# Optimization experiments

Measured on AMD Instinct MI355X. Metric: run time of the kernel, lower is better.

## Reference

```python
import jax, jax.numpy as jnp
import numpy as np

B, S, D = 2, 2048, 2048
H, KVH, HD = 16, 8, 128          # heads, kv heads, head_dim
KVR = 512                        # kv_lora_rank
THETA, ROPE_FACTOR = 10000.0, 40.0
EPS = 1e-5
NEG = -1e9


def _layernorm(x, scale):
    mean = jnp.mean(x, axis=-1, keepdims=True)
    var = jnp.mean(jnp.square(x - mean), axis=-1, keepdims=True)
    return (x - mean) * jax.lax.rsqrt(var + EPS) * scale


def _rope_cos_sin(position_ids):
    # freqs over half the head dim, scaled by rope_factor (as in source)
    freqs = (1.0 / THETA ** (jnp.arange(0, HD, 2, dtype=jnp.float32) / HD)) * ROPE_FACTOR
    ang = position_ids.astype(jnp.float32)[:, None] * freqs[None, :]  # [S, HD//2]
    return jnp.cos(ang)[None, :, None, :], jnp.sin(ang)[None, :, None, :]


def _apply_rope(x, cos, sin):
    # x: [B,S,h,HD] with interleaved (real, imag) pairs
    x_ = x.reshape(*x.shape[:-1], -1, 2)
    xr, xi = x_[..., 0], x_[..., 1]
    out = jnp.stack([xr * cos - xi * sin, xr * sin + xi * cos], axis=-1)
    return out.reshape(x.shape)


def setup_inputs() -> dict:
    key = jax.random.key(0)
    ks = jax.random.split(key, 6)
    std = 0.02
    x = jax.random.normal(ks[0], (B, S, D), jnp.float32)
    wq = jax.random.normal(ks[1], (D, H * 2 * HD), jnp.float32) * std
    wkv_a = jax.random.normal(ks[2], (D, KVR + HD), jnp.float32) * std
    kv_norm_scale = jnp.ones((KVR,), jnp.float32)
    wkv_b = jax.random.normal(ks[3], (KVR, KVH * 2 * HD), jnp.float32) * std
    wo = jax.random.normal(ks[4], (H * HD, D), jnp.float32) * std
    causal = jnp.tril(jnp.ones((S, S), bool))
    attention_mask = jnp.where(causal, 0.0, NEG)[None, None].astype(jnp.float32)
    position_ids = jnp.arange(S, dtype=jnp.int32)
    return {"x": x, "wq": wq, "wkv_a": wkv_a, "kv_norm_scale": kv_norm_scale,
            "wkv_b": wkv_b, "wo": wo, "attention_mask": attention_mask,
            "position_ids": position_ids}


def reference(x, wq, wkv_a, kv_norm_scale, wkv_b, wo, attention_mask, position_ids):
    cos, sin = _rope_cos_sin(position_ids)
    # Q path: low-rank disabled (q_lora_rank=0) -> single projection
    q = (x @ wq).reshape(B, S, H, 2 * HD)
    q_nope, q_pe = q[..., :HD], q[..., HD:]
    q = jnp.concatenate([q_nope, _apply_rope(q_pe, cos, sin)], axis=-1)  # [B,S,H,2HD]
    # KV path: low-rank compression + decoupled rope key
    kv = x @ wkv_a                               # [B,S,KVR+HD]
    kv_c = _layernorm(kv[..., :KVR], kv_norm_scale)
    k_pe = kv[..., KVR:]                         # [B,S,HD]
    kvb = (kv_c @ wkv_b).reshape(B, S, KVH, 2 * HD)
    k_nope, v = kvb[..., :HD], kvb[..., HD:]
    k_pe = _apply_rope(k_pe[:, :, None, :], cos, sin)  # [B,S,1,HD]
    k = jnp.concatenate([k_nope, jnp.broadcast_to(k_pe, (B, S, KVH, HD))], axis=-1)
    # GQA expansion
    rep = H // KVH
    k = jnp.repeat(k, rep, axis=2)
    v = jnp.repeat(v, rep, axis=2)
    scale = HD ** -0.5
    scores = jnp.einsum('bqhd,bkhd->bhqk', q, k) * scale + attention_mask
    probs = jax.nn.softmax(scores, axis=-1)
    attn = jnp.einsum('bhqk,bkhd->bqhd', probs, v).reshape(B, S, H * HD)
    return attn @ wo
```

## Files before the change

### kernel.cpp

```cpp
#include <hip/hip_runtime.h>


typedef __attribute__((ext_vector_type(8))) short short8;
typedef __attribute__((ext_vector_type(4))) float floatx4;
typedef unsigned short u16;
typedef unsigned int u32;

__device__ __forceinline__ float bf2f(u16 u){ u32 x=((u32)u)<<16; return __builtin_bit_cast(float,x); }
__device__ __forceinline__ u16 f2bf(float f){ u32 x=__builtin_bit_cast(u32,f); return (u16)((x + 0x7fffu + ((x>>16)&1u))>>16); }

__device__ __forceinline__ floatx4 mfma16(short8 a, short8 b, floatx4 c){
  return __builtin_amdgcn_mfma_f32_16x16x32_bf16(a,b,c,0,0,0);
}

__device__ __forceinline__ void gl_lds16(const u16* g, u16* l){
  __builtin_amdgcn_global_load_lds((const __attribute__((address_space(1))) void*)g,
                                   (__attribute__((address_space(3))) void*)l, 16, 0, 0);
}

__global__ __launch_bounds__(256)
void k_f2b(const float* __restrict__ in, u16* __restrict__ out, size_t n){
  size_t i = ((size_t)blockIdx.x*256 + threadIdx.x)*4;
  if(i >= n) return;
  float4 v = *(const float4*)(in + i);
  out[i+0] = f2bf(v.x); out[i+1] = f2bf(v.y); out[i+2] = f2bf(v.z); out[i+3] = f2bf(v.w);
}

__global__ void k_transpose(const float* __restrict__ in, u16* __restrict__ out, int K, int N){
  __shared__ u16 tile[32][33];
  const int kb = blockIdx.y*32, nb = blockIdx.x*32;
  const int tx = threadIdx.x, ty = threadIdx.y;
#pragma unroll
  for(int i=0;i<4;i++) tile[ty+i*8][tx] = f2bf(in[(size_t)(kb+ty+i*8)*N + nb + tx]);
  __syncthreads();
#pragma unroll
  for(int i=0;i<4;i++) out[(size_t)(nb+ty+i*8)*K + kb + tx] = tile[tx][ty+i*8];
}

__global__ void k_rope_table(float* __restrict__ cosT, float* __restrict__ sinT){
  int idx = blockIdx.x*256 + threadIdx.x;
  if(idx >= 2048*64) return;
  int p = idx>>6, i = idx&63;
  double freq = pow(10000.0, -(double)(2*i)/128.0) * 40.0;
  float ff = (float)freq;
  float ang = (float)((double)p * (double)ff);
  cosT[idx] = (float)cos((double)ang);
  sinT[idx] = (float)sin((double)ang);
}

template<int OUTF32>
__global__ __launch_bounds__(256)
void k_gemm_bt(const u16* __restrict__ A, const u16* __restrict__ Bt, void* __restrict__ Cout,
               int M, int N, int K){
  __shared__ __align__(16) u16 lsA[128*32];
  __shared__ __align__(16) u16 lsB[128*32];
  const int t = threadIdx.x;
  const int m0 = blockIdx.y*128, n0 = blockIdx.x*128;
  const int wv = t>>6, ln = t&63;
  const int wr = (wv>>1)*64, wc = (wv&1)*64;
  const int fr = ln&15, kh = (ln>>4)*8;
  const int srow = wv*16 + (ln>>2), sk = (ln&3)*8;
  const u16* Ag = A + (size_t)(m0 + srow)*K + sk;
  const u16* Bg = Bt + (size_t)(n0 + srow)*K + sk;
  u16* lA0 = &lsA[wv*512];
  u16* lB0 = &lsB[wv*512];
  floatx4 acc[4][4];
#pragma unroll
  for(int i=0;i<4;i++)
#pragma unroll
    for(int j=0;j<4;j++) acc[i][j] = (floatx4){0.f,0.f,0.f,0.f};
  for(int k0=0;k0<K;k0+=32){
    __syncthreads();
    gl_lds16(Ag + k0,              lA0);
    gl_lds16(Ag + (size_t)64*K + k0, lA0 + 2048);
    gl_lds16(Bg + k0,              lB0);
    gl_lds16(Bg + (size_t)64*K + k0, lB0 + 2048);
    __syncthreads();
    short8 af[4], bf[4];
#pragma unroll
    for(int i=0;i<4;i++) af[i] = *(const short8*)&lsA[(wr + i*16 + fr)*32 + kh];
#pragma unroll
    for(int i=0;i<4;i++) bf[i] = *(const short8*)&lsB[(wc + i*16 + fr)*32 + kh];
#pragma unroll
    for(int mi=0;mi<4;mi++)
#pragma unroll
      for(int ni=0;ni<4;ni++) acc[mi][ni] = mfma16(af[mi], bf[ni], acc[mi][ni]);
  }
  const int r0 = (ln>>4)*4, c0 = ln&15;
#pragma unroll
  for(int mi=0;mi<4;mi++)
#pragma unroll
    for(int ni=0;ni<4;ni++){
      const int row = m0 + wr + mi*16 + r0;
      const int col = n0 + wc + ni*16 + c0;
#pragma unroll
      for(int r=0;r<4;r++){
        float v = acc[mi][ni][r];
        if(OUTF32) ((float*)Cout)[(size_t)(row+r)*N + col] = v;
        else       ((u16*)Cout)[(size_t)(row+r)*N + col] = f2bf(v);
      }
    }
}

__global__ __launch_bounds__(256)
void k_ln_rope(const float* __restrict__ kv, const float* __restrict__ scale,
               const int* __restrict__ pid, const float* __restrict__ cosT,
               const float* __restrict__ sinT, u16* __restrict__ kv_cn, u16* __restrict__ k_pe){
  const int tok = blockIdx.x;
  const int t = threadIdx.x;
  const float* row = kv + (size_t)tok*640;
  float v0 = row[2*t], v1 = row[2*t+1];
  float s = v0+v1, ss = v0*v0+v1*v1;
#pragma unroll
  for(int off=32; off>=1; off>>=1){ s += __shfl_xor(s,off); ss += __shfl_xor(ss,off); }
  __shared__ float red[8];
  if((t&63)==0){ red[t>>6]=s; red[4+(t>>6)]=ss; }
  __syncthreads();
  float S4 = red[0]+red[1]+red[2]+red[3];
  float SS4 = red[4]+red[5]+red[6]+red[7];
  float mean = S4*(1.f/512.f);
  float var = SS4*(1.f/512.f) - mean*mean;
  float inv = rsqrtf(var + 1e-5f);
  kv_cn[(size_t)tok*512 + 2*t]   = f2bf((v0-mean)*inv*scale[2*t]);
  kv_cn[(size_t)tok*512 + 2*t+1] = f2bf((v1-mean)*inv*scale[2*t+1]);
  if(t < 128){
    const int sidx = tok & 2047;
    const int p = pid[sidx];
    const int i = t>>1;
    float c = cosT[p*64+i], sn = sinT[p*64+i];
    float xr = row[512+2*i], xi = row[512+2*i+1];
    float val = (t&1) ? (xr*sn + xi*c) : (xr*c - xi*sn);
    k_pe[(size_t)tok*128 + t] = f2bf(val);
  }
}

__global__ __launch_bounds__(256)
void k_q_rope(const u16* __restrict__ q_raw, const int* __restrict__ pid,
              const float* __restrict__ cosT, const float* __restrict__ sinT,
              u16* __restrict__ q_fin){
  const float QS = (float)(0.08838834764831845 * 1.4426950408889634);
  const int tok = blockIdx.x;
  const int b = tok>>11, sidx = tok&2047;
  const int t = threadIdx.x;
  const int p = pid[sidx];
  const int h = t>>4, seg = t&15;
  const u16* src = q_raw + (size_t)tok*4096 + h*256 + seg*16;
  u16* dst = q_fin + (((size_t)(b*16 + h))*2048 + sidx)*256 + seg*16;
  short8 a = *(const short8*)src;
  short8 bv = *(const short8*)(src+8);
  short8 oa, ob;
  if(seg < 8){
#pragma unroll
    for(int j=0;j<8;j++){
      oa[j] = (short)f2bf(bf2f((u16)a[j])*QS);
      ob[j] = (short)f2bf(bf2f((u16)bv[j])*QS);
    }
  } else {
    const int i0 = seg*8 - 64;
#pragma unroll
    for(int j=0;j<4;j++){
      float c = cosT[p*64 + i0 + j], sn = sinT[p*64 + i0 + j];
      float xr = bf2f((u16)a[2*j]), xi = bf2f((u16)a[2*j+1]);
      oa[2*j]   = (short)f2bf((xr*c - xi*sn)*QS);
      oa[2*j+1] = (short)f2bf((xr*sn + xi*c)*QS);
    }
#pragma unroll
    for(int j=0;j<4;j++){
      float c = cosT[p*64 + i0 + 4 + j], sn = sinT[p*64 + i0 + 4 + j];
      float xr = bf2f((u16)bv[2*j]), xi = bf2f((u16)bv[2*j+1]);
      ob[2*j]   = (short)f2bf((xr*c - xi*sn)*QS);
      ob[2*j+1] = (short)f2bf((xr*sn + xi*c)*QS);
    }
  }
  *(short8*)dst = oa;
  *(short8*)(dst+8) = ob;
}

__global__ __launch_bounds__(256)
void k_build_k(const u16* __restrict__ kvb, const u16* __restrict__ k_pe, u16* __restrict__ k_full){
  const int tok = blockIdx.x;
  const int b = tok>>11, sidx = tok&2047;
  const int t = threadIdx.x;
  const int kh = t>>5, seg = t&31;
  short8 v;
  if(seg < 16) v = *(const short8*)(kvb + (size_t)tok*2048 + kh*256 + seg*8);
  else         v = *(const short8*)(k_pe + (size_t)tok*128 + (seg-16)*8);
  *(short8*)(k_full + (((size_t)(b*8 + kh))*2048 + sidx)*256 + seg*8) = v;
}

__global__ void k_v_t(const u16* __restrict__ kvb, u16* __restrict__ v_t){
  __shared__ u16 tile[32][33];
  const int sb = blockIdx.x*32, hb = blockIdx.y*32;
  const int bk = blockIdx.z;
  const int b = bk>>3, kh = bk&7;
  const int tx = threadIdx.x, ty = threadIdx.y;
#pragma unroll
  for(int i=0;i<4;i++){
    int sidx = sb + ty + i*8;
    tile[ty+i*8][tx] = kvb[((size_t)(b*2048 + sidx))*2048 + kh*256 + 128 + hb + tx];
  }
  __syncthreads();
#pragma unroll
  for(int i=0;i<4;i++){
    int hd = hb + ty + i*8;
    v_t[(((size_t)bk*64 + blockIdx.x)*128 + hd)*32 + tx] = tile[tx][ty+i*8];
  }
}

__global__ __launch_bounds__(256, 3)
void k_attn(const u16* __restrict__ q_fin, const u16* __restrict__ k_full,
            const u16* __restrict__ v_t, u16* __restrict__ attn){
  __shared__ __align__(16) u16 lsK[2*8192];
  __shared__ __align__(16) u16 lsP[4*16*40];
  const int blk = blockIdx.x;
  const int kvh = blk&7;
  const int bb  = (blk>>3)&1;
  const int qr  = blk>>4;
  const int qt  = 31 - (qr>>1);
  const int h   = kvh*2 + (qr&1);
  const int t = threadIdx.x, wv = t>>6, ln = t&63;
  const int fq = ln&15, gq = ln>>4;
  const u16* kbase = k_full + ((size_t)(bb*8 + kvh))*2048*256;
  const u16* vbase = v_t + ((size_t)(bb*8 + kvh))*128*2048;
  u16* Pw = &lsP[wv*16*40];

  int soff[4];
#pragma unroll
  for(int s4=0;s4<4;s4++){
    int o = s4*4096 + wv*1024 + ln*16;
    int row = o>>9, colb = o&511;
    soff[s4] = row*512 + (colb ^ ((row&7)<<4));
  }
  const int swz = (fq&7)<<4;
  int cb[8];
#pragma unroll
  for(int c=0;c<8;c++) cb[c] = (gq*16 + c*64) ^ swz;
  const int rowb = fq*512;
  const u16* vfp = vbase + (size_t)fq*32 + gq*8;

  const int last = 2*qt + 1;
  short8 qf[8];
  const u16* qb = q_fin + (((size_t)(bb*16 + h))*2048 + qt*64 + wv*16 + fq)*256;
#pragma unroll
  for(int c=0;c<8;c++) qf[c] = *(const short8*)(qb + c*32 + gq*8);
  floatx4 oacc[8];
#pragma unroll
  for(int ii=0;ii<8;ii++) oacc[ii] = (floatx4){0.f,0.f,0.f,0.f};
  float mprev = -3e38f, lsum = 0.f;

#pragma unroll
  for(int s4=0;s4<4;s4++)
    gl_lds16((const u16*)((const char*)kbase + soff[s4]), &lsK[s4*2048 + wv*512]);
  __syncthreads();

  int cur = 0;
  for(int kt=0; kt<=last; kt++){
    if(kt < last){
      const char* ktile = (const char*)kbase + (size_t)(kt+1)*16384;
      u16* kdst = &lsK[(cur^1)*8192];
#pragma unroll
      for(int s4=0;s4<4;s4++)
        gl_lds16((const u16*)(ktile + soff[s4]), kdst + s4*2048 + wv*512);
    }
    short8 vf[8];
#pragma unroll
    for(int hs=0;hs<8;hs++)
      vf[hs] = *(const short8*)(vfp + (size_t)kt*4096 + hs*512);

    const char* Kc = (const char*)lsK + cur*16384;
    floatx4 sc[2];
#pragma unroll
    for(int ns=0;ns<2;ns++) sc[ns] = (floatx4){0.f,0.f,0.f,0.f};
#pragma unroll
    for(int ns=0;ns<2;ns++){
#pragma unroll
      for(int c=0;c<8;c++){
        short8 kf = *(const short8*)(Kc + ns*8192 + rowb + cb[c]);
        sc[ns] = mfma16(kf, qf[c], sc[ns]);
      }
    }
    if(kt >= 2*qt){
      const int off = (kt - 2*qt)*32;
      const int qloc = wv*16 + fq;
#pragma unroll
      for(int ns=0;ns<2;ns++)
#pragma unroll
        for(int r=0;r<4;r++)
          if(off + ns*16 + gq*4 + r > qloc) sc[ns][r] = -1e30f;
    }
    float mloc = -3e38f;
#pragma unroll
    for(int ns=0;ns<2;ns++)
#pragma unroll
      for(int r=0;r<4;r++) mloc = fmaxf(mloc, sc[ns][r]);
    mloc = fmaxf(mloc, __shfl_xor(mloc, 16));
    mloc = fmaxf(mloc, __shfl_xor(mloc, 32));
    if(__any(mloc > mprev + 8.f)){
      const float mn = fmaxf(mprev, mloc);
      const float alpha = exp2f(mprev - mn);
      lsum *= alpha;
      float alphaO[4];
#pragma unroll
      for(int r=0;r<4;r++) alphaO[r] = __shfl(alpha, gq*4 + r);
#pragma unroll
      for(int hs=0;hs<8;hs++)
#pragma unroll
        for(int r=0;r<4;r++) oacc[hs][r] *= alphaO[r];
      mprev = mn;
    }
    float ps = 0.f;
#pragma unroll
    for(int ns=0;ns<2;ns++)
#pragma unroll
      for(int r=0;r<4;r++){
        float p = exp2f(sc[ns][r] - mprev);
        sc[ns][r] = p;
        ps += p;
      }
    ps += __shfl_xor(ps, 16);
    ps += __shfl_xor(ps, 32);
    lsum += ps;

#pragma unroll
    for(int ns=0;ns<2;ns++){
      u32 p01, p23;
      asm("v_cvt_pk_bf16_f32 %0, %1, %2" : "=v"(p01) : "v"(sc[ns][0]), "v"(sc[ns][1]));
      asm("v_cvt_pk_bf16_f32 %0, %1, %2" : "=v"(p23) : "v"(sc[ns][2]), "v"(sc[ns][3]));
      uint2 pk; pk.x = p01; pk.y = p23;
      *(uint2*)&Pw[fq*40 + ns*16 + gq*4] = pk;
    }
    __builtin_amdgcn_s_waitcnt(0xC07F);

    short8 pa = *(const short8*)&Pw[fq*40 + gq*8];
#pragma unroll
    for(int hs=0;hs<8;hs++)
      oacc[hs] = mfma16(pa, vf[hs], oacc[hs]);

    __syncthreads();
    cur ^= 1;
  }
  const float inv = 1.f / lsum;
  float invO[4];
#pragma unroll
  for(int r=0;r<4;r++) invO[r] = __shfl(inv, gq*4 + r);
#pragma unroll
  for(int hs=0;hs<8;hs++)
#pragma unroll
    for(int r=0;r<4;r++){
      const int qi = qt*64 + wv*16 + gq*4 + r;
      attn[(((size_t)(bb*2048 + qi))*16 + h)*128 + hs*16 + fq] = f2bf(oacc[hs][r]*invO[r]);
    }
}

extern "C" void kernel_launch(void* const* d_in, const int* in_sizes, int n_in,
                              void* d_out, int out_size, void* d_ws, size_t ws_size,
                              hipStream_t stream){
  const float* x    = (const float*)d_in[0];
  const float* wq   = (const float*)d_in[1];
  const float* wkva = (const float*)d_in[2];
  const float* kvsc = (const float*)d_in[3];
  const float* wkvb = (const float*)d_in[4];
  const float* wo   = (const float*)d_in[5];
  const int* pid  = (const int*)d_in[7];
  float* out = (float*)d_out;

  char* w = (char*)d_ws;
  size_t off = 0;
  auto alloc = [&](size_t bytes)->void*{
    void* p = (void*)(w + off);
    off += (bytes + 255) & ~(size_t)255;
    return p;
  };
  u16*   x_bf   = (u16*)alloc((size_t)4096*2048*2);
  u16*   wq_t   = (u16*)alloc((size_t)4096*2048*2);
  u16*   wkva_t = (u16*)alloc((size_t)640*2048*2);
  u16*   wkvb_t = (u16*)alloc((size_t)2048*512*2);
  u16*   wo_t   = (u16*)alloc((size_t)2048*2048*2);
  float* cosT   = (float*)alloc((size_t)2048*64*4);
  float* sinT   = (float*)alloc((size_t)2048*64*4);
  u16*   q_raw  = (u16*)alloc((size_t)4096*4096*2);
  float* kvf    = (float*)alloc((size_t)4096*640*4);
  u16*   kv_cn  = (u16*)alloc((size_t)4096*512*2);
  u16*   k_pe   = (u16*)alloc((size_t)4096*128*2);
  u16*   kvb    = (u16*)alloc((size_t)4096*2048*2);
  u16*   q_fin  = (u16*)alloc((size_t)4096*4096*2);
  u16*   k_full = (u16*)alloc((size_t)2*8*2048*256*2);
  u16*   v_t    = (u16*)alloc((size_t)2*8*128*2048*2);
  u16*   attn   = (u16*)alloc((size_t)4096*2048*2);

  k_f2b<<<8192, 256, 0, stream>>>(x, x_bf, (size_t)4096*2048);
  k_transpose<<<dim3(128, 64), dim3(32,8), 0, stream>>>(wq,   wq_t,   2048, 4096);
  k_transpose<<<dim3(20,  64), dim3(32,8), 0, stream>>>(wkva, wkva_t, 2048, 640);
  k_transpose<<<dim3(64,  16), dim3(32,8), 0, stream>>>(wkvb, wkvb_t, 512,  2048);
  k_transpose<<<dim3(64,  64), dim3(32,8), 0, stream>>>(wo,   wo_t,   2048, 2048);
  k_rope_table<<<512, 256, 0, stream>>>(cosT, sinT);

  k_gemm_bt<0><<<dim3(32, 32), 256, 0, stream>>>(x_bf, wq_t, q_raw, 4096, 4096, 2048);
  k_gemm_bt<1><<<dim3(5,  32), 256, 0, stream>>>(x_bf, wkva_t, kvf, 4096, 640, 2048);
  k_ln_rope<<<4096, 256, 0, stream>>>(kvf, kvsc, pid, cosT, sinT, kv_cn, k_pe);
  k_gemm_bt<0><<<dim3(16, 32), 256, 0, stream>>>(kv_cn, wkvb_t, kvb, 4096, 2048, 512);
  k_q_rope<<<4096, 256, 0, stream>>>(q_raw, pid, cosT, sinT, q_fin);
  k_build_k<<<4096, 256, 0, stream>>>(kvb, k_pe, k_full);
  k_v_t<<<dim3(64, 4, 16), dim3(32,8), 0, stream>>>(kvb, v_t);
  k_attn<<<1024, 256, 0, stream>>>(q_fin, k_full, v_t, attn);
  k_gemm_bt<1><<<dim3(16, 32), 256, 0, stream>>>(attn, wo_t, out, 4096, 2048, 2048);
}
```

Measured before the change: 517.9 us.

## Use 2-wave attention blocks with two 16-row query tiles per wave

The attention kernel now runs 128 threads (2 waves) per block instead of 4. Each wave handles 32 query rows as two 16-row sub-tiles, so each K fragment read from LDS and each V fragment loaded from global memory feeds twice as many MFMAs. The block-to-tile mapping also changes to interleave short and long causal query tiles (0..7, 31..24, 8..15, 23..16), which should balance load across the grid. The cost is roughly double the accumulator and Q registers per wave and a lower occupancy bound, which may hurt latency hiding.

```diff
diff --git a/kernel.cpp b/kernel.cpp
--- a/kernel.cpp
+++ b/kernel.cpp
@@ -207,29 +207,37 @@
   }
 }
 
-__global__ __launch_bounds__(256, 3)
+__global__ __launch_bounds__(128, 2)
 void k_attn(const u16* __restrict__ q_fin, const u16* __restrict__ k_full,
             const u16* __restrict__ v_t, u16* __restrict__ attn){
   __shared__ __align__(16) u16 lsK[2*8192];
-  __shared__ __align__(16) u16 lsP[4*16*40];
+  __shared__ __align__(16) u16 lsP[2*32*40];
   const int blk = blockIdx.x;
   const int kvh = blk&7;
-  const int bb  = (blk>>3)&1;
-  const int qr  = blk>>4;
-  const int qt  = 31 - (qr>>1);
-  const int h   = kvh*2 + (qr&1);
+  const int i  = blk>>3;
+  const int j  = i>>5;
+  const int mm = i&31;
+  const int s  = mm>>2;
+  int qt;
+  if(j==0)      qt = s;
+  else if(j==1) qt = 31 - s;
+  else if(j==2) qt = 8 + s;
+  else          qt = 23 - s;
+  const int bb = (mm>>1)&1;
+  const int hp = mm&1;
+  const int h  = kvh*2 + hp;
   const int t = threadIdx.x, wv = t>>6, ln = t&63;
   const int fq = ln&15, gq = ln>>4;
   const u16* kbase = k_full + ((size_t)(bb*8 + kvh))*2048*256;
   const u16* vbase = v_t + ((size_t)(bb*8 + kvh))*128*2048;
-  u16* Pw = &lsP[wv*16*40];
-
-  int soff[4];
-#pragma unroll
-  for(int s4=0;s4<4;s4++){
-    int o = s4*4096 + wv*1024 + ln*16;
+  u16* Pw = &lsP[wv*32*40];
+
+  int soff[8];
+#pragma unroll
+  for(int s8=0;s8<8;s8++){
+    int o = s8*2048 + t*16;
     int row = o>>9, colb = o&511;
-    soff[s4] = row*512 + (colb ^ ((row&7)<<4));
+    soff[s8] = row*512 + (colb ^ ((row&7)<<4));
   }
   const int swz = (fq&7)<<4;
   int cb[8];
@@ -239,18 +247,23 @@
   const u16* vfp = vbase + (size_t)fq*32 + gq*8;
 
   const int last = 2*qt + 1;
-  short8 qf[8];
-  const u16* qb = q_fin + (((size_t)(bb*16 + h))*2048 + qt*64 + wv*16 + fq)*256;
-#pragma unroll
-  for(int c=0;c<8;c++) qf[c] = *(const short8*)(qb + c*32 + gq*8);
-  floatx4 oacc[8];
-#pragma unroll
-  for(int ii=0;ii<8;ii++) oacc[ii] = (floatx4){0.f,0.f,0.f,0.f};
-  float mprev = -3e38f, lsum = 0.f;
-
-#pragma unroll
-  for(int s4=0;s4<4;s4++)
-    gl_lds16((const u16*)((const char*)kbase + soff[s4]), &lsK[s4*2048 + wv*512]);
+  short8 qf[2][8];
+#pragma unroll
+  for(int m=0;m<2;m++){
+    const u16* qb = q_fin + (((size_t)(bb*16 + h))*2048 + qt*64 + wv*32 + m*16 + fq)*256;
+#pragma unroll
+    for(int c=0;c<8;c++) qf[m][c] = *(const short8*)(qb + c*32 + gq*8);
+  }
+  floatx4 oacc[2][8];
+#pragma unroll
+  for(int m=0;m<2;m++)
+#pragma unroll
+    for(int ii=0;ii<8;ii++) oacc[m][ii] = (floatx4){0.f,0.f,0.f,0.f};
+  float mprev0 = -3e38f, mprev1 = -3e38f, lsum0 = 0.f, lsum1 = 0.f;
+
+#pragma unroll
+  for(int s8=0;s8<8;s8++)
+    gl_lds16((const u16*)((const char*)kbase + soff[s8]), &lsK[s8*1024 + wv*512]);
   __syncthreads();
 
   int cur = 0;
@@ -259,8 +272,8 @@
       const char* ktile = (const char*)kbase + (size_t)(kt+1)*16384;
       u16* kdst = &lsK[(cur^1)*8192];
 #pragma unroll
-      for(int s4=0;s4<4;s4++)
-        gl_lds16((const u16*)(ktile + soff[s4]), kdst + s4*2048 + wv*512);
+      for(int s8=0;s8<8;s8++)
+        gl_lds16((const u16*)(ktile + soff[s8]), kdst + s8*1024 + wv*512);
     }
     short8 vf[8];
 #pragma unroll
@@ -268,88 +281,102 @@
       vf[hs] = *(const short8*)(vfp + (size_t)kt*4096 + hs*512);
 
     const char* Kc = (const char*)lsK + cur*16384;
-    floatx4 sc[2];
-#pragma unroll
-    for(int ns=0;ns<2;ns++) sc[ns] = (floatx4){0.f,0.f,0.f,0.f};
+    floatx4 sc[2][2];
+#pragma unroll
+    for(int m=0;m<2;m++)
+#pragma unroll
+      for(int ns=0;ns<2;ns++) sc[m][ns] = (floatx4){0.f,0.f,0.f,0.f};
 #pragma unroll
     for(int ns=0;ns<2;ns++){
 #pragma unroll
       for(int c=0;c<8;c++){
         short8 kf = *(const short8*)(Kc + ns*8192 + rowb + cb[c]);
-        sc[ns] = mfma16(kf, qf[c], sc[ns]);
+        sc[0][ns] = mfma16(kf, qf[0][c], sc[0][ns]);
+        sc[1][ns] = mfma16(kf, qf[1][c], sc[1][ns]);
       }
     }
     if(kt >= 2*qt){
       const int off = (kt - 2*qt)*32;
-      const int qloc = wv*16 + fq;
-#pragma unroll
-      for(int ns=0;ns<2;ns++)
-#pragma unroll
-        for(int r=0;r<4;r++)
-          if(off + ns*16 + gq*4 + r > qloc) sc[ns][r] = -1e30f;
-    }
-    float mloc = -3e38f;
+#pragma unroll
+      for(int m=0;m<2;m++){
+        const int qloc = wv*32 + m*16 + fq;
+#pragma unroll
+        for(int ns=0;ns<2;ns++)
+#pragma unroll
+          for(int r=0;r<4;r++)
+            if(off + ns*16 + gq*4 + r > qloc) sc[m][ns][r] = -1e30f;
+      }
+    }
+    float ml0 = -3e38f, ml1 = -3e38f;
 #pragma unroll
     for(int ns=0;ns<2;ns++)
 #pragma unroll
-      for(int r=0;r<4;r++) mloc = fmaxf(mloc, sc[ns][r]);
-    mloc = fmaxf(mloc, __shfl_xor(mloc, 16));
-    mloc = fmaxf(mloc, __shfl_xor(mloc, 32));
-    if(__any(mloc > mprev + 8.f)){
-      const float mn = fmaxf(mprev, mloc);
-      const float alpha = exp2f(mprev - mn);
-      lsum *= alpha;
-      float alphaO[4];
-#pragma unroll
-      for(int r=0;r<4;r++) alphaO[r] = __shfl(alpha, gq*4 + r);
+      for(int r=0;r<4;r++){ ml0 = fmaxf(ml0, sc[0][ns][r]); ml1 = fmaxf(ml1, sc[1][ns][r]); }
+    ml0 = fmaxf(ml0, __shfl_xor(ml0, 16)); ml0 = fmaxf(ml0, __shfl_xor(ml0, 32));
+    ml1 = fmaxf(ml1, __shfl_xor(ml1, 16)); ml1 = fmaxf(ml1, __shfl_xor(ml1, 32));
+    if(__any((ml0 > mprev0 + 8.f) || (ml1 > mprev1 + 8.f))){
+      const float mn0 = fmaxf(mprev0, ml0), mn1 = fmaxf(mprev1, ml1);
+      const float a0 = exp2f(mprev0 - mn0), a1 = exp2f(mprev1 - mn1);
+      lsum0 *= a0; lsum1 *= a1;
+      float aO0[4], aO1[4];
+#pragma unroll
+      for(int r=0;r<4;r++){ aO0[r] = __shfl(a0, gq*4 + r); aO1[r] = __shfl(a1, gq*4 + r); }
 #pragma unroll
       for(int hs=0;hs<8;hs++)
 #pragma unroll
-        for(int r=0;r<4;r++) oacc[hs][r] *= alphaO[r];
-      mprev = mn;
-    }
-    float ps = 0.f;
+        for(int r=0;r<4;r++){ oacc[0][hs][r] *= aO0[r]; oacc[1][hs][r] *= aO1[r]; }
+      mprev0 = mn0; mprev1 = mn1;
+    }
+    float ps0 = 0.f, ps1 = 0.f;
 #pragma unroll
     for(int ns=0;ns<2;ns++)
 #pragma unroll
       for(int r=0;r<4;r++){
-        float p = exp2f(sc[ns][r] - mprev);
-        sc[ns][r] = p;
-        ps += p;
-      }
-    ps += __shfl_xor(ps, 16);
-    ps += __shfl_xor(ps, 32);
-    lsum += ps;
-
-#pragma unroll
-    for(int ns=0;ns<2;ns++){
-      u32 p01, p23;
-      asm("v_cvt_pk_bf16_f32 %0, %1, %2" : "=v"(p01) : "v"(sc[ns][0]), "v"(sc[ns][1]));
-      asm("v_cvt_pk_bf16_f32 %0, %1, %2" : "=v"(p23) : "v"(sc[ns][2]), "v"(sc[ns][3]));
-      uint2 pk; pk.x = p01; pk.y = p23;
-      *(uint2*)&Pw[fq*40 + ns*16 + gq*4] = pk;
-    }
+        float p0 = exp2f(sc[0][ns][r] - mprev0);
+        float p1 = exp2f(sc[1][ns][r] - mprev1);
+        sc[0][ns][r] = p0; sc[1][ns][r] = p1;
+        ps0 += p0; ps1 += p1;
+      }
+    ps0 += __shfl_xor(ps0, 16); ps0 += __shfl_xor(ps0, 32);
+    ps1 += __shfl_xor(ps1, 16); ps1 += __shfl_xor(ps1, 32);
+    lsum0 += ps0; lsum1 += ps1;
+
+#pragma unroll
+    for(int m=0;m<2;m++)
+#pragma unroll
+      for(int ns=0;ns<2;ns++){
+        u32 p01, p23;
+        asm("v_cvt_pk_bf16_f32 %0, %1, %2" : "=v"(p01) : "v"(sc[m][ns][0]), "v"(sc[m][ns][1]));
+        asm("v_cvt_pk_bf16_f32 %0, %1, %2" : "=v"(p23) : "v"(sc[m][ns][2]), "v"(sc[m][ns][3]));
+        uint2 pk; pk.x = p01; pk.y = p23;
+        *(uint2*)&Pw[(m*16 + fq)*40 + ns*16 + gq*4] = pk;
+      }
     __builtin_amdgcn_s_waitcnt(0xC07F);
 
-    short8 pa = *(const short8*)&Pw[fq*40 + gq*8];
-#pragma unroll
-    for(int hs=0;hs<8;hs++)
-      oacc[hs] = mfma16(pa, vf[hs], oacc[hs]);
-
+#pragma unroll
+    for(int m=0;m<2;m++){
+      short8 pa = *(const short8*)&Pw[(m*16 + fq)*40 + gq*8];
+#pragma unroll
+      for(int hs=0;hs<8;hs++)
+        oacc[m][hs] = mfma16(pa, vf[hs], oacc[m][hs]);
+    }
     __syncthreads();
     cur ^= 1;
   }
-  const float inv = 1.f / lsum;
-  float invO[4];
-#pragma unroll
-  for(int r=0;r<4;r++) invO[r] = __shfl(inv, gq*4 + r);
-#pragma unroll
-  for(int hs=0;hs<8;hs++)
-#pragma unroll
-    for(int r=0;r<4;r++){
-      const int qi = qt*64 + wv*16 + gq*4 + r;
-      attn[(((size_t)(bb*2048 + qi))*16 + h)*128 + hs*16 + fq] = f2bf(oacc[hs][r]*invO[r]);
-    }
+  const float i0 = 1.f / lsum0, i1 = 1.f / lsum1;
+  float iO0[4], iO1[4];
+#pragma unroll
+  for(int r=0;r<4;r++){ iO0[r] = __shfl(i0, gq*4 + r); iO1[r] = __shfl(i1, gq*4 + r); }
+#pragma unroll
+  for(int m=0;m<2;m++)
+#pragma unroll
+    for(int hs=0;hs<8;hs++)
+#pragma unroll
+      for(int r=0;r<4;r++){
+        const int qi = qt*64 + wv*32 + m*16 + gq*4 + r;
+        float sc_ = (m==0) ? iO0[r] : iO1[r];
+        attn[(((size_t)(bb*2048 + qi))*16 + h)*128 + hs*16 + fq] = f2bf(oacc[m][hs][r]*sc_);
+      }
 }
 
 extern "C" void kernel_launch(void* const* d_in, const int* in_sizes, int n_in,
@@ -402,6 +429,6 @@
   k_q_rope<<<4096, 256, 0, stream>>>(q_raw, pid, cosT, sinT, q_fin);
   k_build_k<<<4096, 256, 0, stream>>>(kvb, k_pe, k_full);
   k_v_t<<<dim3(64, 4, 16), dim3(32,8), 0, stream>>>(kvb, v_t);
-  k_attn<<<1024, 256, 0, stream>>>(q_fin, k_full, v_t, attn);
+  k_attn<<<1024, 128, 0, stream>>>(q_fin, k_full, v_t, attn);
   k_gemm_bt<1><<<dim3(16, 32), 256, 0, stream>>>(attn, wo_t, out, 4096, 2048, 2048);
 }
```

Result: no change. 520.0 us (+0.4%).
